# Kernel tuning notes

Hardware: AMD Instinct MI355X
Metric: run time of the kernel (lower is better)

Reference implementation:

```python
import jax, jax.numpy as jnp
import numpy as np

WINDOW = 4
EPS = 1e-5


def setup_inputs() -> dict:
    key = jax.random.key(0)
    ks = jax.random.split(key, 12)
    B, T, D = 2, 4096, 1024
    H = D // 2
    s = 0.02
    return {
        "x": jax.random.normal(ks[0], (B, T, D), dtype=jnp.float32),
        # tension_net: Linear(2D -> D/2), SiLU, Linear(D/2 -> 1). Weights stored [in, out].
        "w1": jax.random.normal(ks[1], (2 * D, H), dtype=jnp.float32) * s,
        "b1": jnp.zeros((H,), dtype=jnp.float32),
        "w2": jax.random.normal(ks[2], (H, 1), dtype=jnp.float32) * s,
        "b2": jnp.zeros((1,), dtype=jnp.float32),
        # wv: Linear(D -> D)
        "wv_w": jax.random.normal(ks[3], (D, D), dtype=jnp.float32) * s,
        "wv_b": jnp.zeros((D,), dtype=jnp.float32),
        # merge: Linear(2D -> D)
        "merge_w": jax.random.normal(ks[4], (2 * D, D), dtype=jnp.float32) * s,
        "merge_b": jnp.zeros((D,), dtype=jnp.float32),
        # LayerNorm(D)
        "gamma": jnp.ones((D,), dtype=jnp.float32),
        "beta": jnp.zeros((D,), dtype=jnp.float32),
    }


def reference(x, w1, b1, w2, b2, wv_w, wv_b, merge_w, merge_b, gamma, beta):
    B, T, D = x.shape
    W = WINDOW
    # Causal sliding-window neighbor gather: nb[:, t, w] = x[:, t-w-1] if t-w-1 >= 0 else 0.
    idx = jnp.arange(T)[:, None] - jnp.arange(W)[None, :] - 1          # [T, W]
    valid = (idx >= 0)                                                  # [T, W]
    nb = jnp.take(x, jnp.clip(idx, 0, None), axis=1)                   # [B, T, W, D]
    nb = jnp.where(valid[None, :, :, None], nb, jnp.zeros((), x.dtype))
    # Pairwise tension gate: tiny MLP on [h_t, nb].
    h_t = jnp.broadcast_to(x[:, :, None, :], (B, T, W, D))
    pair = jnp.concatenate([h_t, nb], axis=-1)                          # [B, T, W, 2D]
    hid = jax.nn.silu(jnp.einsum('btwe,eh->btwh', pair, w1) + b1)       # [B, T, W, D/2]
    tau = jax.nn.sigmoid((jnp.einsum('btwh,ho->btwo', hid, w2) + b2)[..., 0])  # [B, T, W]
    # Value projection of neighbors (note: zero-padded neighbors still get wv bias, matching torch).
    v = jnp.einsum('btwd,de->btwe', nb, wv_w) + wv_b                    # [B, T, W, D]
    msg = jnp.einsum('btw,btwd->btd', tau, v)                           # [B, T, D]
    # Merge + LayerNorm.
    y = jnp.einsum('bte,ed->btd', jnp.concatenate([x, msg], axis=-1), merge_w) + merge_b
    mu = jnp.mean(y, axis=-1, keepdims=True)
    var = jnp.mean(jnp.square(y - mu), axis=-1, keepdims=True)
    y = (y - mu) * jax.lax.rsqrt(var + EPS) * gamma + beta
    return y
```

## Files before the change

### kernel.cpp

```cpp
#include <hip/hip_runtime.h>
#include <hip/hip_bf16.h>

#define TT 4096
#define TD 1024
#define TM 8192
#define CN 3072
#define EPS 1e-5f

typedef __bf16 bf16;
typedef __bf16 bf16x4 __attribute__((ext_vector_type(4)));
typedef __bf16 bf16x8 __attribute__((ext_vector_type(8)));
typedef float  f32x4  __attribute__((ext_vector_type(4)));

#define GLOBAL_AS __attribute__((address_space(1)))
#define LDS_AS    __attribute__((address_space(3)))

__global__ __launch_bounds__(256) void prep_kernel(const float* __restrict__ x,
                                                   const float* __restrict__ w1,
                                                   const float* __restrict__ wv_w,
                                                   const float* __restrict__ wv_b,
                                                   const float* __restrict__ merge_w,
                                                   bf16* __restrict__ Xbf,
                                                   bf16* __restrict__ BigBT,
                                                   bf16* __restrict__ Amb,
                                                   bf16* __restrict__ WvBf,
                                                   float* __restrict__ cvecP) {
    __shared__ float tile[32][33];
    int b = blockIdx.x;
    const int tid = threadIdx.x;

    if (b < 16) {
        const int j = (b & 3) * 256 + tid;
        const int e0 = (b >> 2) * 256;
        const float* col = merge_w + (size_t)(1024 + e0) * 1024 + j;
        float acc = 0.f;
#pragma unroll 32
        for (int e = 0; e < 256; ++e) acc += wv_b[e0 + e] * col[(size_t)e * 1024];
        cvecP[(b >> 2) * 1024 + j] = acc;
        return;
    }
    b -= 16;
    if (b < 8192) {
        int i = b * 256 + tid;
        float4 v = ((const float4*)x)[i];
        bf16x4 o; o[0] = (bf16)v.x; o[1] = (bf16)v.y; o[2] = (bf16)v.z; o[3] = (bf16)v.w;
        *(bf16x4*)(Xbf + (size_t)i * 4) = o;
        return;
    }
    b -= 8192;

    const float* src; bf16* dst; int srcN, tilesX, dstOff;
    if (b < 512)       {            src = w1;                        srcN = 512;  tilesX = 16; dst = BigBT; dstOff = 0;    }
    else if (b < 1024) { b -= 512;  src = w1 + (size_t)1024 * 512;   srcN = 512;  tilesX = 16; dst = BigBT; dstOff = 512;  }
    else if (b < 2048) { b -= 1024; src = merge_w;                   srcN = 1024; tilesX = 32; dst = BigBT; dstOff = 2048; }
    else if (b < 3072) { b -= 2048; src = merge_w + (size_t)1024 * 1024; srcN = 1024; tilesX = 32; dst = Amb; dstOff = 0; }
    else {
        b -= 3072;
        int i = b * 256 + tid;
        float4 v = ((const float4*)wv_w)[i];
        bf16x4 o; o[0] = (bf16)v.x; o[1] = (bf16)v.y; o[2] = (bf16)v.z; o[3] = (bf16)v.w;
        *(bf16x4*)(WvBf + (size_t)i * 4) = o;
        return;
    }
    int n0 = (b % tilesX) * 32, k0 = (b / tilesX) * 32;
    int tx = tid & 31, ty = tid >> 5;
#pragma unroll
    for (int r = 0; r < 32; r += 8)
        tile[ty + r][tx] = src[(size_t)(k0 + ty + r) * srcN + n0 + tx];
    __syncthreads();
#pragma unroll
    for (int r = 0; r < 32; r += 8)
        dst[(size_t)(dstOff + n0 + ty + r) * 1024 + k0 + tx] = (bf16)tile[tx][ty + r];
}

__global__ __launch_bounds__(256) void wprime_kernel(const bf16* __restrict__ Amb,
                                                     const bf16* __restrict__ WvBf,
                                                     bf16* __restrict__ Wout,
                                                     const float* __restrict__ cvecP,
                                                     float* __restrict__ cvec) {
    int b = blockIdx.x;
    if (b == 256) {
        int j = threadIdx.x * 4;
        float4 s0 = *(const float4*)(cvecP + j);
        float4 s1 = *(const float4*)(cvecP + 1024 + j);
        float4 s2 = *(const float4*)(cvecP + 2048 + j);
        float4 s3 = *(const float4*)(cvecP + 3072 + j);
        float4 o = {s0.x + s1.x + s2.x + s3.x, s0.y + s1.y + s2.y + s3.y,
                    s0.z + s1.z + s2.z + s3.z, s0.w + s1.w + s2.w + s3.w};
        *(float4*)(cvec + j) = o;
        return;
    }
    __shared__ bf16 As[64 * 64];
    __shared__ bf16 Bs[64 * 64];
    const int m0 = (b >> 4) * 64;
    const int n0 = (b & 15) * 64;
    const int tid = threadIdx.x;
    const int wave = tid >> 6, lane = tid & 63;
    const int wr = (wave >> 1) * 32, wc = (wave & 1) * 32;
    const int lrow = lane & 15, cbase = lane >> 4;
    const int sw = lrow & 7;

    f32x4 acc[2][2] = {};

    for (int k0 = 0; k0 < 1024; k0 += 64) {
        __syncthreads();
#pragma unroll
        for (int c = 0; c < 2; ++c) {
            int e = (c * 256 + tid) * 8;
            int row = e >> 6;
            int q = (e >> 3) & 7;
            int gcol = ((q ^ (row & 7)) << 3);
            const bf16* ga = Amb  + (size_t)(m0 + row) * 1024 + k0 + gcol;
            const bf16* gb = WvBf + (size_t)(n0 + row) * 1024 + k0 + gcol;
            __builtin_amdgcn_global_load_lds((const GLOBAL_AS void*)ga,
                                             (LDS_AS void*)(As + e), 16, 0, 0);
            __builtin_amdgcn_global_load_lds((const GLOBAL_AS void*)gb,
                                             (LDS_AS void*)(Bs + e), 16, 0, 0);
        }
        __syncthreads();

#pragma unroll
        for (int kk = 0; kk < 2; ++kk) {
            const int qo = ((cbase + kk * 4) ^ sw) << 3;
            bf16x8 af[2], bfr[2];
#pragma unroll
            for (int i = 0; i < 2; ++i) {
                af[i]  = *(const bf16x8*)(As + (wr + i * 16 + lrow) * 64 + qo);
                bfr[i] = *(const bf16x8*)(Bs + (wc + i * 16 + lrow) * 64 + qo);
            }
#pragma unroll
            for (int i = 0; i < 2; ++i)
#pragma unroll
                for (int j = 0; j < 2; ++j)
                    acc[i][j] = __builtin_amdgcn_mfma_f32_16x16x32_bf16(af[i], bfr[j], acc[i][j], 0, 0, 0);
        }
    }

    const int lr = (lane >> 4) * 4, lc = lane & 15;
#pragma unroll
    for (int i = 0; i < 2; ++i)
#pragma unroll
        for (int j = 0; j < 2; ++j)
#pragma unroll
            for (int r = 0; r < 4; ++r)
                Wout[(size_t)(m0 + wr + i * 16 + lr + r) * 1024 + (n0 + wc + j * 16 + lc)]
                    = (bf16)acc[i][j][r];
}

__global__ __launch_bounds__(256, 2) void gemm_big(const bf16* __restrict__ A,
                                                   const bf16* __restrict__ BT,
                                                   bf16* __restrict__ C) {
    __shared__ bf16 SMEM[28672];
    bf16* As = SMEM;
    bf16* Bs = SMEM + 16384;
    const int NB = 3072, K = 1024;

    int bx = blockIdx.x, by = blockIdx.y;
    {
        int L = by * 32 + bx;
        int xcd = L & 7, idx = L >> 3;
        by = xcd * 4 + (idx >> 5);
        bx = idx & 31;
    }
    const int m0 = by * 256;
    const int n0 = bx * 96;
    const int tid = threadIdx.x;
    const int wave = tid >> 6, lane = tid & 63;
    const int wr = wave * 64;
    const int lrow = lane & 15, cbase = lane >> 4;
    const int sw = lrow & 7;

    f32x4 acc[4][6] = {};

    for (int k0 = 0; k0 < K; k0 += 64) {
        __syncthreads();
#pragma unroll
        for (int c = 0; c < 11; ++c) {
            if (c < 8) {
                int e = (c * 256 + tid) * 8;
                int row = e >> 6;
                int q = (e >> 3) & 7;
                int gcol = ((q ^ (row & 7)) << 3);
                const bf16* ga = A + (size_t)(m0 + row) * K + k0 + gcol;
                __builtin_amdgcn_global_load_lds((const GLOBAL_AS void*)ga,
                                                 (LDS_AS void*)(As + e), 16, 0, 0);
            } else {
                int e = ((c - 8) * 256 + tid) * 8;
                int row = e >> 6;
                int q = (e >> 3) & 7;
                int gcol = ((q ^ (row & 7)) << 3);
                const bf16* gb = BT + (size_t)(n0 + row) * K + k0 + gcol;
                __builtin_amdgcn_global_load_lds((const GLOBAL_AS void*)gb,
                                                 (LDS_AS void*)(Bs + e), 16, 0, 0);
            }
        }
        __syncthreads();

#pragma unroll
        for (int kk = 0; kk < 2; ++kk) {
            const int qo = ((cbase + kk * 4) ^ sw) << 3;
            bf16x8 af[4], bfr[6];
#pragma unroll
            for (int i = 0; i < 4; ++i)
                af[i] = *(const bf16x8*)(As + (wr + i * 16 + lrow) * 64 + qo);
#pragma unroll
            for (int j = 0; j < 6; ++j)
                bfr[j] = *(const bf16x8*)(Bs + (j * 16 + lrow) * 64 + qo);
#pragma unroll
            for (int i = 0; i < 4; ++i)
#pragma unroll
                for (int j = 0; j < 6; ++j)
                    acc[i][j] = __builtin_amdgcn_mfma_f32_16x16x32_bf16(af[i], bfr[j], acc[i][j], 0, 0, 0);
        }
    }

    __syncthreads();
    bf16* ep = SMEM + wave * 6656;
    const int lr = (lane >> 4) * 4, lc = lane & 15;
#pragma unroll
    for (int i = 0; i < 4; ++i)
#pragma unroll
        for (int j = 0; j < 6; ++j)
#pragma unroll
            for (int r = 0; r < 4; ++r)
                ep[(i * 16 + lr + r) * 104 + (j * 16 + lc)] = (bf16)acc[i][j][r];
    __syncthreads();

    bf16* Cw = C + (size_t)(m0 + wr) * NB + n0;
#pragma unroll
    for (int p = 0; p < 8; ++p) {
        int R = p * 8 + (lane >> 3);
        int Ccol = (lane & 7) * 8;
        bf16x8 v = *(const bf16x8*)(ep + R * 104 + Ccol);
        *(bf16x8*)(Cw + (size_t)R * NB + Ccol) = v;
    }
#pragma unroll
    for (int p = 0; p < 4; ++p) {
        int R = p * 16 + (lane >> 2);
        int Ccol = 64 + (lane & 3) * 8;
        bf16x8 v = *(const bf16x8*)(ep + R * 104 + Ccol);
        *(bf16x8*)(Cw + (size_t)R * NB + Ccol) = v;
    }
}

__global__ __launch_bounds__(256) void final_kernel(const bf16* __restrict__ C,
                                                    const float* __restrict__ b1,
                                                    const float* __restrict__ b2,
                                                    const float* __restrict__ w2,
                                                    const float* __restrict__ cvec,
                                                    const float* __restrict__ merge_b,
                                                    const float* __restrict__ gamma,
                                                    const float* __restrict__ beta,
                                                    float* __restrict__ out) {
    const int wave = threadIdx.x >> 6, lane = threadIdx.x & 63;
    const int row = blockIdx.x * 4 + wave;
    const int t = row & (TT - 1);
    const bf16* Crow = C + (size_t)row * CN;

    const int h0 = lane * 8;
    bf16x8 u8 = *(const bf16x8*)(Crow + h0);
    float4 b1a = *(const float4*)(b1 + h0), b1b = *(const float4*)(b1 + h0 + 4);
    float4 w2a = *(const float4*)(w2 + h0), w2b = *(const float4*)(w2 + h0 + 4);
    float u[8] = {(float)u8[0] + b1a.x, (float)u8[1] + b1a.y,
                  (float)u8[2] + b1a.z, (float)u8[3] + b1a.w,
                  (float)u8[4] + b1b.x, (float)u8[5] + b1b.y,
                  (float)u8[6] + b1b.z, (float)u8[7] + b1b.w};
    const float w2v[8] = {w2a.x, w2a.y, w2a.z, w2a.w, w2b.x, w2b.y, w2b.z, w2b.w};

    float partial[4];
#pragma unroll
    for (int w = 0; w < 4; ++w) {
        float p = 0.f;
        if (t >= w + 1) {
            bf16x8 v8 = *(const bf16x8*)(C + (size_t)(row - w - 1) * CN + 512 + h0);
#pragma unroll
            for (int k = 0; k < 8; ++k) {
                float z = u[k] + (float)v8[k];
                p += (z / (1.f + __expf(-z))) * w2v[k];
            }
        } else {
#pragma unroll
            for (int k = 0; k < 8; ++k) {
                float z = u[k];
                p += (z / (1.f + __expf(-z))) * w2v[k];
            }
        }
        partial[w] = p;
    }
#pragma unroll
    for (int w = 0; w < 4; ++w)
#pragma unroll
        for (int off = 1; off < 64; off <<= 1)
            partial[w] += __shfl_xor(partial[w], off, 64);

    const float bias2 = b2[0];
    float taus[4];
#pragma unroll
    for (int w = 0; w < 4; ++w)
        taus[w] = 1.f / (1.f + __expf(-(partial[w] + bias2)));
    const float tsum = taus[0] + taus[1] + taus[2] + taus[3];

    const int d0 = lane * 16;
    bf16x8 y1a = *(const bf16x8*)(Crow + 2048 + d0);
    bf16x8 y1b = *(const bf16x8*)(Crow + 2048 + d0 + 8);
    float v[16];
#pragma unroll
    for (int k = 0; k < 8; ++k) { v[k] = (float)y1a[k]; v[8 + k] = (float)y1b[k]; }
#pragma unroll
    for (int q = 0; q < 4; ++q) {
        float4 cv = *(const float4*)(cvec + d0 + q * 4);
        float4 mb = *(const float4*)(merge_b + d0 + q * 4);
        v[q*4+0] += tsum * cv.x + mb.x; v[q*4+1] += tsum * cv.y + mb.y;
        v[q*4+2] += tsum * cv.z + mb.z; v[q*4+3] += tsum * cv.w + mb.w;
    }
#pragma unroll
    for (int w = 0; w < 4; ++w) {
        if (t >= w + 1) {
            const bf16* Pn = C + (size_t)(row - w - 1) * CN + 1024 + d0;
            bf16x8 pa = *(const bf16x8*)Pn;
            bf16x8 pb = *(const bf16x8*)(Pn + 8);
#pragma unroll
            for (int k = 0; k < 8; ++k) {
                v[k] += taus[w] * (float)pa[k];
                v[8 + k] += taus[w] * (float)pb[k];
            }
        }
    }

    float s = 0.f, ss = 0.f;
#pragma unroll
    for (int k = 0; k < 16; ++k) { s += v[k]; ss += v[k] * v[k]; }
#pragma unroll
    for (int off = 1; off < 64; off <<= 1) {
        s  += __shfl_xor(s, off, 64);
        ss += __shfl_xor(ss, off, 64);
    }
    const float mu = s * (1.f / TD);
    const float var = ss * (1.f / TD) - mu * mu;
    const float r = rsqrtf(var + EPS);

#pragma unroll
    for (int q = 0; q < 4; ++q) {
        float4 g  = *(const float4*)(gamma + d0 + q * 4);
        float4 bt = *(const float4*)(beta + d0 + q * 4);
        float4 o;
        o.x = (v[q*4+0] - mu) * r * g.x + bt.x;
        o.y = (v[q*4+1] - mu) * r * g.y + bt.y;
        o.z = (v[q*4+2] - mu) * r * g.z + bt.z;
        o.w = (v[q*4+3] - mu) * r * g.w + bt.w;
        *(float4*)(out + (size_t)row * TD + d0 + q * 4) = o;
    }
}

extern "C" void kernel_launch(void* const* d_in, const int* in_sizes, int n_in,
                              void* d_out, int out_size, void* d_ws, size_t ws_size,
                              hipStream_t stream) {
    const float* x       = (const float*)d_in[0];
    const float* w1      = (const float*)d_in[1];
    const float* b1      = (const float*)d_in[2];
    const float* w2      = (const float*)d_in[3];
    const float* b2      = (const float*)d_in[4];
    const float* wv_w    = (const float*)d_in[5];
    const float* wv_b    = (const float*)d_in[6];
    const float* merge_w = (const float*)d_in[7];
    const float* merge_b = (const float*)d_in[8];
    const float* gamma   = (const float*)d_in[9];
    const float* beta    = (const float*)d_in[10];
    float* out = (float*)d_out;

    char* ws = (char*)d_ws;
    bf16*  Xbf   = (bf16*)ws;  ws += (size_t)TM * 1024 * 2;
    bf16*  BigBT = (bf16*)ws;  ws += (size_t)CN * 1024 * 2;
    bf16*  Amb   = (bf16*)ws;  ws += (size_t)1024 * 1024 * 2;
    bf16*  WvBf  = (bf16*)ws;  ws += (size_t)1024 * 1024 * 2;
    float* cvecP = (float*)ws; ws += (size_t)4 * 1024 * 4;
    float* cvec  = (float*)ws; ws += (size_t)1024 * 4;
    bf16*  Cbuf  = (bf16*)ws;

    prep_kernel<<<12304, 256, 0, stream>>>(x, w1, wv_w, wv_b, merge_w,
                                           Xbf, BigBT, Amb, WvBf, cvecP);

    wprime_kernel<<<257, 256, 0, stream>>>(Amb, WvBf, BigBT + (size_t)1024 * 1024,
                                           cvecP, cvec);

    gemm_big<<<dim3(32, 32), 256, 0, stream>>>(Xbf, BigBT, Cbuf);

    final_kernel<<<TM / 4, 256, 0, stream>>>(Cbuf, b1, b2, w2, cvec, merge_b,
                                             gamma, beta, out);
}
```

Baseline: 195.1 us.

## Fuse all stages into one cooperative persistent kernel with grid syncs

Merges the prep, weight-product, main GEMM and final LayerNorm stages into a single cooperative kernel of 512 persistent blocks that loop over work units, with grid-wide barriers between stages. The cvec partial-sum reduction now happens inside the final stage, so the separate reduction block goes away. The aim is to remove the gaps between kernel launches. In exchange, every stage shares one 56KB LDS allocation and a fixed grid, which may lower occupancy for the light stages, and grid.sync adds its own cost. A fallback to separate launches is kept in case the cooperative launch fails.

New measurement: 409.8 us. 110% more time.

```diff
diff --git a/kernel.cpp b/kernel.cpp
--- a/kernel.cpp
+++ b/kernel.cpp
@@ -1,5 +1,8 @@
 #include <hip/hip_runtime.h>
 #include <hip/hip_bf16.h>
+#include <hip/hip_cooperative_groups.h>
+
+namespace cg = cooperative_groups;
 
 #define TT 4096
 #define TD 1024
@@ -15,20 +18,18 @@
 #define GLOBAL_AS __attribute__((address_space(1)))
 #define LDS_AS    __attribute__((address_space(3)))
 
-__global__ __launch_bounds__(256) void prep_kernel(const float* __restrict__ x,
-                                                   const float* __restrict__ w1,
-                                                   const float* __restrict__ wv_w,
-                                                   const float* __restrict__ wv_b,
-                                                   const float* __restrict__ merge_w,
-                                                   bf16* __restrict__ Xbf,
-                                                   bf16* __restrict__ BigBT,
-                                                   bf16* __restrict__ Amb,
-                                                   bf16* __restrict__ WvBf,
-                                                   float* __restrict__ cvecP) {
-    __shared__ float tile[32][33];
-    int b = blockIdx.x;
+__device__ __forceinline__ void prep_unit(int b, char* smem,
+                                          const float* __restrict__ x,
+                                          const float* __restrict__ w1,
+                                          const float* __restrict__ wv_w,
+                                          const float* __restrict__ wv_b,
+                                          const float* __restrict__ merge_w,
+                                          bf16* __restrict__ Xbf,
+                                          bf16* __restrict__ BigBT,
+                                          bf16* __restrict__ Amb,
+                                          bf16* __restrict__ WvBf,
+                                          float* __restrict__ cvecP) {
     const int tid = threadIdx.x;
-
     if (b < 16) {
         const int j = (b & 3) * 256 + tid;
         const int e0 = (b >> 2) * 256;
@@ -48,20 +49,19 @@
         return;
     }
     b -= 8192;
-
-    const float* src; bf16* dst; int srcN, tilesX, dstOff;
-    if (b < 512)       {            src = w1;                        srcN = 512;  tilesX = 16; dst = BigBT; dstOff = 0;    }
-    else if (b < 1024) { b -= 512;  src = w1 + (size_t)1024 * 512;   srcN = 512;  tilesX = 16; dst = BigBT; dstOff = 512;  }
-    else if (b < 2048) { b -= 1024; src = merge_w;                   srcN = 1024; tilesX = 32; dst = BigBT; dstOff = 2048; }
-    else if (b < 3072) { b -= 2048; src = merge_w + (size_t)1024 * 1024; srcN = 1024; tilesX = 32; dst = Amb; dstOff = 0; }
-    else {
-        b -= 3072;
-        int i = b * 256 + tid;
+    if (b >= 3072) {
+        int i = (b - 3072) * 256 + tid;
         float4 v = ((const float4*)wv_w)[i];
         bf16x4 o; o[0] = (bf16)v.x; o[1] = (bf16)v.y; o[2] = (bf16)v.z; o[3] = (bf16)v.w;
         *(bf16x4*)(WvBf + (size_t)i * 4) = o;
         return;
     }
+    const float* src; bf16* dst; int srcN, tilesX, dstOff;
+    if (b < 512)       {           src = w1;                        srcN = 512;  tilesX = 16; dst = BigBT; dstOff = 0;    }
+    else if (b < 1024) { b -= 512; src = w1 + (size_t)1024 * 512;   srcN = 512;  tilesX = 16; dst = BigBT; dstOff = 512;  }
+    else if (b < 2048) { b -= 1024; src = merge_w;                  srcN = 1024; tilesX = 32; dst = BigBT; dstOff = 2048; }
+    else               { b -= 2048; src = merge_w + (size_t)1024 * 1024; srcN = 1024; tilesX = 32; dst = Amb; dstOff = 0; }
+    float (*tile)[33] = (float(*)[33])smem;
     int n0 = (b % tilesX) * 32, k0 = (b / tilesX) * 32;
     int tx = tid & 31, ty = tid >> 5;
 #pragma unroll
@@ -71,27 +71,15 @@
 #pragma unroll
     for (int r = 0; r < 32; r += 8)
         dst[(size_t)(dstOff + n0 + ty + r) * 1024 + k0 + tx] = (bf16)tile[tx][ty + r];
-}
-
-__global__ __launch_bounds__(256) void wprime_kernel(const bf16* __restrict__ Amb,
-                                                     const bf16* __restrict__ WvBf,
-                                                     bf16* __restrict__ Wout,
-                                                     const float* __restrict__ cvecP,
-                                                     float* __restrict__ cvec) {
-    int b = blockIdx.x;
-    if (b == 256) {
-        int j = threadIdx.x * 4;
-        float4 s0 = *(const float4*)(cvecP + j);
-        float4 s1 = *(const float4*)(cvecP + 1024 + j);
-        float4 s2 = *(const float4*)(cvecP + 2048 + j);
-        float4 s3 = *(const float4*)(cvecP + 3072 + j);
-        float4 o = {s0.x + s1.x + s2.x + s3.x, s0.y + s1.y + s2.y + s3.y,
-                    s0.z + s1.z + s2.z + s3.z, s0.w + s1.w + s2.w + s3.w};
-        *(float4*)(cvec + j) = o;
-        return;
-    }
-    __shared__ bf16 As[64 * 64];
-    __shared__ bf16 Bs[64 * 64];
+    __syncthreads();
+}
+
+__device__ __forceinline__ void wprime_unit(int b, char* smem,
+                                            const bf16* __restrict__ Amb,
+                                            const bf16* __restrict__ WvBf,
+                                            bf16* __restrict__ Wout) {
+    bf16* As = (bf16*)smem;
+    bf16* Bs = (bf16*)smem + 4096;
     const int m0 = (b >> 4) * 64;
     const int n0 = (b & 15) * 64;
     const int tid = threadIdx.x;
@@ -135,6 +123,7 @@
                     acc[i][j] = __builtin_amdgcn_mfma_f32_16x16x32_bf16(af[i], bfr[j], acc[i][j], 0, 0, 0);
         }
     }
+    __syncthreads();
 
     const int lr = (lane >> 4) * 4, lc = lane & 15;
 #pragma unroll
@@ -147,21 +136,17 @@
                     = (bf16)acc[i][j][r];
 }
 
-__global__ __launch_bounds__(256, 2) void gemm_big(const bf16* __restrict__ A,
-                                                   const bf16* __restrict__ BT,
-                                                   bf16* __restrict__ C) {
-    __shared__ bf16 SMEM[28672];
-    bf16* As = SMEM;
-    bf16* Bs = SMEM + 16384;
+__device__ __forceinline__ void gemm_tile(int tb, char* smem,
+                                          const bf16* __restrict__ A,
+                                          const bf16* __restrict__ BT,
+                                          bf16* __restrict__ C) {
+    bf16* As = (bf16*)smem;
+    bf16* Bs = (bf16*)smem + 16384;
     const int NB = 3072, K = 1024;
 
-    int bx = blockIdx.x, by = blockIdx.y;
-    {
-        int L = by * 32 + bx;
-        int xcd = L & 7, idx = L >> 3;
-        by = xcd * 4 + (idx >> 5);
-        bx = idx & 31;
-    }
+    const int xcd = tb & 7, idx = tb >> 3;
+    const int by = xcd * 4 + (idx >> 5);
+    const int bx = idx & 31;
     const int m0 = by * 256;
     const int n0 = bx * 96;
     const int tid = threadIdx.x;
@@ -215,7 +200,7 @@
     }
 
     __syncthreads();
-    bf16* ep = SMEM + wave * 6656;
+    bf16* ep = (bf16*)smem + wave * 6656;
     const int lr = (lane >> 4) * 4, lc = lane & 15;
 #pragma unroll
     for (int i = 0; i < 4; ++i)
@@ -243,17 +228,18 @@
     }
 }
 
-__global__ __launch_bounds__(256) void final_kernel(const bf16* __restrict__ C,
-                                                    const float* __restrict__ b1,
-                                                    const float* __restrict__ b2,
-                                                    const float* __restrict__ w2,
-                                                    const float* __restrict__ cvec,
-                                                    const float* __restrict__ merge_b,
-                                                    const float* __restrict__ gamma,
-                                                    const float* __restrict__ beta,
-                                                    float* __restrict__ out) {
+__device__ __forceinline__ void final_unit(int b,
+                                           const bf16* __restrict__ C,
+                                           const float* __restrict__ b1,
+                                           const float* __restrict__ b2,
+                                           const float* __restrict__ w2,
+                                           const float* __restrict__ cvecP,
+                                           const float* __restrict__ merge_b,
+                                           const float* __restrict__ gamma,
+                                           const float* __restrict__ beta,
+                                           float* __restrict__ out) {
     const int wave = threadIdx.x >> 6, lane = threadIdx.x & 63;
-    const int row = blockIdx.x * 4 + wave;
+    const int row = b * 4 + wave;
     const int t = row & (TT - 1);
     const bf16* Crow = C + (size_t)row * CN;
 
@@ -308,10 +294,16 @@
     for (int k = 0; k < 8; ++k) { v[k] = (float)y1a[k]; v[8 + k] = (float)y1b[k]; }
 #pragma unroll
     for (int q = 0; q < 4; ++q) {
-        float4 cv = *(const float4*)(cvec + d0 + q * 4);
-        float4 mb = *(const float4*)(merge_b + d0 + q * 4);
-        v[q*4+0] += tsum * cv.x + mb.x; v[q*4+1] += tsum * cv.y + mb.y;
-        v[q*4+2] += tsum * cv.z + mb.z; v[q*4+3] += tsum * cv.w + mb.w;
+        const int d = d0 + q * 4;
+        float4 c0 = *(const float4*)(cvecP + d);
+        float4 c1 = *(const float4*)(cvecP + 1024 + d);
+        float4 c2 = *(const float4*)(cvecP + 2048 + d);
+        float4 c3 = *(const float4*)(cvecP + 3072 + d);
+        float4 mb = *(const float4*)(merge_b + d);
+        v[q*4+0] += tsum * (c0.x + c1.x + c2.x + c3.x) + mb.x;
+        v[q*4+1] += tsum * (c0.y + c1.y + c2.y + c3.y) + mb.y;
+        v[q*4+2] += tsum * (c0.z + c1.z + c2.z + c3.z) + mb.z;
+        v[q*4+3] += tsum * (c0.w + c1.w + c2.w + c3.w) + mb.w;
     }
 #pragma unroll
     for (int w = 0; w < 4; ++w) {
@@ -341,15 +333,68 @@
 
 #pragma unroll
     for (int q = 0; q < 4; ++q) {
-        float4 g  = *(const float4*)(gamma + d0 + q * 4);
-        float4 bt = *(const float4*)(beta + d0 + q * 4);
+        const int d = d0 + q * 4;
+        float4 g  = *(const float4*)(gamma + d);
+        float4 bt = *(const float4*)(beta + d);
         float4 o;
         o.x = (v[q*4+0] - mu) * r * g.x + bt.x;
         o.y = (v[q*4+1] - mu) * r * g.y + bt.y;
         o.z = (v[q*4+2] - mu) * r * g.z + bt.z;
         o.w = (v[q*4+3] - mu) * r * g.w + bt.w;
-        *(float4*)(out + (size_t)row * TD + d0 + q * 4) = o;
-    }
+        *(float4*)(out + (size_t)row * TD + d) = o;
+    }
+}
+
+__global__ __launch_bounds__(256, 2) void mega_kernel(
+        const float* x, const float* w1, const float* b1, const float* w2,
+        const float* b2, const float* wv_w, const float* wv_b,
+        const float* merge_w, const float* merge_b, const float* gamma,
+        const float* beta, bf16* Xbf, bf16* BigBT, bf16* Amb, bf16* WvBf,
+        float* cvecP, bf16* Cbuf, float* out) {
+    cg::grid_group grid = cg::this_grid();
+    __shared__ __align__(16) char smem[57344];
+
+    for (int b = blockIdx.x; b < 12304; b += 512)
+        prep_unit(b, smem, x, w1, wv_w, wv_b, merge_w, Xbf, BigBT, Amb, WvBf, cvecP);
+    grid.sync();
+
+    if (blockIdx.x < 256)
+        wprime_unit(blockIdx.x, smem, Amb, WvBf, BigBT + (size_t)1024 * 1024);
+    grid.sync();
+
+    for (int tb = blockIdx.x; tb < 1024; tb += 512)
+        gemm_tile(tb, smem, Xbf, BigBT, Cbuf);
+    grid.sync();
+
+    for (int b = blockIdx.x; b < 2048; b += 512)
+        final_unit(b, Cbuf, b1, b2, w2, cvecP, merge_b, gamma, beta, out);
+}
+
+__global__ __launch_bounds__(256) void prep_kernel(
+        const float* x, const float* w1, const float* wv_w, const float* wv_b,
+        const float* merge_w, bf16* Xbf, bf16* BigBT, bf16* Amb, bf16* WvBf,
+        float* cvecP) {
+    __shared__ __align__(16) char smem[4224];
+    prep_unit(blockIdx.x, smem, x, w1, wv_w, wv_b, merge_w, Xbf, BigBT, Amb, WvBf, cvecP);
+}
+
+__global__ __launch_bounds__(256) void wprime_kernel(
+        const bf16* Amb, const bf16* WvBf, bf16* Wout) {
+    __shared__ __align__(16) char smem[16384];
+    wprime_unit(blockIdx.x, smem, Amb, WvBf, Wout);
+}
+
+__global__ __launch_bounds__(256, 2) void gemm_kernel(
+        const bf16* A, const bf16* BT, bf16* C) {
+    __shared__ __align__(16) char smem[57344];
+    gemm_tile(blockIdx.x, smem, A, BT, C);
+}
+
+__global__ __launch_bounds__(256) void final_kernel(
+        const bf16* C, const float* b1, const float* b2, const float* w2,
+        const float* cvecP, const float* merge_b, const float* gamma,
+        const float* beta, float* out) {
+    final_unit(blockIdx.x, C, b1, b2, w2, cvecP, merge_b, gamma, beta, out);
 }
 
 extern "C" void kernel_launch(void* const* d_in, const int* in_sizes, int n_in,
@@ -374,17 +419,23 @@
     bf16*  Amb   = (bf16*)ws;  ws += (size_t)1024 * 1024 * 2;
     bf16*  WvBf  = (bf16*)ws;  ws += (size_t)1024 * 1024 * 2;
     float* cvecP = (float*)ws; ws += (size_t)4 * 1024 * 4;
-    float* cvec  = (float*)ws; ws += (size_t)1024 * 4;
     bf16*  Cbuf  = (bf16*)ws;
 
-    prep_kernel<<<12304, 256, 0, stream>>>(x, w1, wv_w, wv_b, merge_w,
-                                           Xbf, BigBT, Amb, WvBf, cvecP);
-
-    wprime_kernel<<<257, 256, 0, stream>>>(Amb, WvBf, BigBT + (size_t)1024 * 1024,
-                                           cvecP, cvec);
-
-    gemm_big<<<dim3(32, 32), 256, 0, stream>>>(Xbf, BigBT, Cbuf);
-
-    final_kernel<<<TM / 4, 256, 0, stream>>>(Cbuf, b1, b2, w2, cvec, merge_b,
-                                             gamma, beta, out);
-}
+    void* args[] = {(void*)&x, (void*)&w1, (void*)&b1, (void*)&w2, (void*)&b2,
+                    (void*)&wv_w, (void*)&wv_b, (void*)&merge_w, (void*)&merge_b,
+                    (void*)&gamma, (void*)&beta,
+                    (void*)&Xbf, (void*)&BigBT, (void*)&Amb, (void*)&WvBf,
+                    (void*)&cvecP, (void*)&Cbuf, (void*)&out};
+    hipError_t err = hipLaunchCooperativeKernel((void*)mega_kernel,
+                                                dim3(512), dim3(256),
+                                                args, 0, stream);
+    if (err != hipSuccess) {
+        (void)hipGetLastError();
+        prep_kernel<<<12304, 256, 0, stream>>>(x, w1, wv_w, wv_b, merge_w,
+                                               Xbf, BigBT, Amb, WvBf, cvecP);
+        wprime_kernel<<<256, 256, 0, stream>>>(Amb, WvBf, BigBT + (size_t)1024 * 1024);
+        gemm_kernel<<<1024, 256, 0, stream>>>(Xbf, BigBT, Cbuf);
+        final_kernel<<<2048, 256, 0, stream>>>(Cbuf, b1, b2, w2, cvecP, merge_b,
+                                               gamma, beta, out);
+    }
+}
```

## Rebalance prep work: move x conversion and cvec partials into wprime GEMM launch

Applied to the files above, without the earlier changes.

Weight transposes stay in the prep kernel. The x-to-bf16 conversion and the wv_b·merge_w partial sums move into the W' GEMM launch, so that small GEMM overlaps with bandwidth-bound conversion blocks and the prep kernel shrinks. The final cvec reduction is folded into final_kernel, which now reads the four partials directly. Other changes: the big GEMM uses a 1D grid, one epilogue barrier is dropped, and final_kernel rows are remapped for XCD locality. Removing the barrier after the per-wave LDS epilogue relies on each wave reading back only its own region.

Result: slower. 200.8 us (+2.9%).

```diff
diff --git a/kernel.cpp b/kernel.cpp
--- a/kernel.cpp
+++ b/kernel.cpp
@@ -15,21 +15,54 @@
 #define GLOBAL_AS __attribute__((address_space(1)))
 #define LDS_AS    __attribute__((address_space(3)))
 
-__global__ __launch_bounds__(256) void prep_kernel(const float* __restrict__ x,
-                                                   const float* __restrict__ w1,
+__global__ __launch_bounds__(256) void prep_kernel(const float* __restrict__ w1,
                                                    const float* __restrict__ wv_w,
-                                                   const float* __restrict__ wv_b,
                                                    const float* __restrict__ merge_w,
-                                                   bf16* __restrict__ Xbf,
                                                    bf16* __restrict__ BigBT,
                                                    bf16* __restrict__ Amb,
-                                                   bf16* __restrict__ WvBf,
-                                                   float* __restrict__ cvecP) {
+                                                   bf16* __restrict__ WvBf) {
     __shared__ float tile[32][33];
     int b = blockIdx.x;
     const int tid = threadIdx.x;
 
-    if (b < 16) {
+    if (b >= 3072) {
+        int i = (b - 3072) * 256 + tid;
+        float4 v = ((const float4*)wv_w)[i];
+        bf16x4 o; o[0] = (bf16)v.x; o[1] = (bf16)v.y; o[2] = (bf16)v.z; o[3] = (bf16)v.w;
+        *(bf16x4*)(WvBf + (size_t)i * 4) = o;
+        return;
+    }
+    const float* src; bf16* dst; int srcN, tilesX, dstOff;
+    if (b < 512)       {            src = w1;                        srcN = 512;  tilesX = 16; dst = BigBT; dstOff = 0;    }
+    else if (b < 1024) { b -= 512;  src = w1 + (size_t)1024 * 512;   srcN = 512;  tilesX = 16; dst = BigBT; dstOff = 512;  }
+    else if (b < 2048) { b -= 1024; src = merge_w;                   srcN = 1024; tilesX = 32; dst = BigBT; dstOff = 2048; }
+    else               { b -= 2048; src = merge_w + (size_t)1024 * 1024; srcN = 1024; tilesX = 32; dst = Amb; dstOff = 0; }
+    int n0 = (b % tilesX) * 32, k0 = (b / tilesX) * 32;
+    int tx = tid & 31, ty = tid >> 5;
+#pragma unroll
+    for (int r = 0; r < 32; r += 8)
+        tile[ty + r][tx] = src[(size_t)(k0 + ty + r) * srcN + n0 + tx];
+    __syncthreads();
+#pragma unroll
+    for (int r = 0; r < 32; r += 8)
+        dst[(size_t)(dstOff + n0 + ty + r) * 1024 + k0 + tx] = (bf16)tile[tx][ty + r];
+}
+
+__global__ __launch_bounds__(256) void aux_kernel(const float* __restrict__ x,
+                                                  const float* __restrict__ merge_w,
+                                                  const float* __restrict__ wv_b,
+                                                  const bf16* __restrict__ Amb,
+                                                  const bf16* __restrict__ WvBf,
+                                                  bf16* __restrict__ Wout,
+                                                  bf16* __restrict__ Xbf,
+                                                  float* __restrict__ cvecP) {
+    __shared__ bf16 As[64 * 64];
+    __shared__ bf16 Bs[64 * 64];
+    int b = blockIdx.x;
+    const int tid = threadIdx.x;
+
+    if (b >= 8448) {
+        b -= 8448;
         const int j = (b & 3) * 256 + tid;
         const int e0 = (b >> 2) * 256;
         const float* col = merge_w + (size_t)(1024 + e0) * 1024 + j;
@@ -39,62 +72,15 @@
         cvecP[(b >> 2) * 1024 + j] = acc;
         return;
     }
-    b -= 16;
-    if (b < 8192) {
-        int i = b * 256 + tid;
+    if (b >= 256) {
+        int i = (b - 256) * 256 + tid;
         float4 v = ((const float4*)x)[i];
         bf16x4 o; o[0] = (bf16)v.x; o[1] = (bf16)v.y; o[2] = (bf16)v.z; o[3] = (bf16)v.w;
         *(bf16x4*)(Xbf + (size_t)i * 4) = o;
         return;
     }
-    b -= 8192;
-
-    const float* src; bf16* dst; int srcN, tilesX, dstOff;
-    if (b < 512)       {            src = w1;                        srcN = 512;  tilesX = 16; dst = BigBT; dstOff = 0;    }
-    else if (b < 1024) { b -= 512;  src = w1 + (size_t)1024 * 512;   srcN = 512;  tilesX = 16; dst = BigBT; dstOff = 512;  }
-    else if (b < 2048) { b -= 1024; src = merge_w;                   srcN = 1024; tilesX = 32; dst = BigBT; dstOff = 2048; }
-    else if (b < 3072) { b -= 2048; src = merge_w + (size_t)1024 * 1024; srcN = 1024; tilesX = 32; dst = Amb; dstOff = 0; }
-    else {
-        b -= 3072;
-        int i = b * 256 + tid;
-        float4 v = ((const float4*)wv_w)[i];
-        bf16x4 o; o[0] = (bf16)v.x; o[1] = (bf16)v.y; o[2] = (bf16)v.z; o[3] = (bf16)v.w;
-        *(bf16x4*)(WvBf + (size_t)i * 4) = o;
-        return;
-    }
-    int n0 = (b % tilesX) * 32, k0 = (b / tilesX) * 32;
-    int tx = tid & 31, ty = tid >> 5;
-#pragma unroll
-    for (int r = 0; r < 32; r += 8)
-        tile[ty + r][tx] = src[(size_t)(k0 + ty + r) * srcN + n0 + tx];
-    __syncthreads();
-#pragma unroll
-    for (int r = 0; r < 32; r += 8)
-        dst[(size_t)(dstOff + n0 + ty + r) * 1024 + k0 + tx] = (bf16)tile[tx][ty + r];
-}
-
-__global__ __launch_bounds__(256) void wprime_kernel(const bf16* __restrict__ Amb,
-                                                     const bf16* __restrict__ WvBf,
-                                                     bf16* __restrict__ Wout,
-                                                     const float* __restrict__ cvecP,
-                                                     float* __restrict__ cvec) {
-    int b = blockIdx.x;
-    if (b == 256) {
-        int j = threadIdx.x * 4;
-        float4 s0 = *(const float4*)(cvecP + j);
-        float4 s1 = *(const float4*)(cvecP + 1024 + j);
-        float4 s2 = *(const float4*)(cvecP + 2048 + j);
-        float4 s3 = *(const float4*)(cvecP + 3072 + j);
-        float4 o = {s0.x + s1.x + s2.x + s3.x, s0.y + s1.y + s2.y + s3.y,
-                    s0.z + s1.z + s2.z + s3.z, s0.w + s1.w + s2.w + s3.w};
-        *(float4*)(cvec + j) = o;
-        return;
-    }
-    __shared__ bf16 As[64 * 64];
-    __shared__ bf16 Bs[64 * 64];
     const int m0 = (b >> 4) * 64;
     const int n0 = (b & 15) * 64;
-    const int tid = threadIdx.x;
     const int wave = tid >> 6, lane = tid & 63;
     const int wr = (wave >> 1) * 32, wc = (wave & 1) * 32;
     const int lrow = lane & 15, cbase = lane >> 4;
@@ -147,21 +133,18 @@
                     = (bf16)acc[i][j][r];
 }
 
-__global__ __launch_bounds__(256, 2) void gemm_big(const bf16* __restrict__ A,
-                                                   const bf16* __restrict__ BT,
-                                                   bf16* __restrict__ C) {
+__global__ __launch_bounds__(256, 2) void gemm_kernel(const bf16* __restrict__ A,
+                                                      const bf16* __restrict__ BT,
+                                                      bf16* __restrict__ C) {
     __shared__ bf16 SMEM[28672];
     bf16* As = SMEM;
     bf16* Bs = SMEM + 16384;
     const int NB = 3072, K = 1024;
 
-    int bx = blockIdx.x, by = blockIdx.y;
-    {
-        int L = by * 32 + bx;
-        int xcd = L & 7, idx = L >> 3;
-        by = xcd * 4 + (idx >> 5);
-        bx = idx & 31;
-    }
+    const int tb = blockIdx.x;
+    const int xcd = tb & 7, idx = tb >> 3;
+    const int by = xcd * 4 + (idx >> 5);
+    const int bx = idx & 31;
     const int m0 = by * 256;
     const int n0 = bx * 96;
     const int tid = threadIdx.x;
@@ -224,7 +207,6 @@
 #pragma unroll
             for (int r = 0; r < 4; ++r)
                 ep[(i * 16 + lr + r) * 104 + (j * 16 + lc)] = (bf16)acc[i][j][r];
-    __syncthreads();
 
     bf16* Cw = C + (size_t)(m0 + wr) * NB + n0;
 #pragma unroll
@@ -247,13 +229,14 @@
                                                     const float* __restrict__ b1,
                                                     const float* __restrict__ b2,
                                                     const float* __restrict__ w2,
-                                                    const float* __restrict__ cvec,
+                                                    const float* __restrict__ cvecP,
                                                     const float* __restrict__ merge_b,
                                                     const float* __restrict__ gamma,
                                                     const float* __restrict__ beta,
                                                     float* __restrict__ out) {
+    const int g = (blockIdx.x & 7) * 256 + (blockIdx.x >> 3);
     const int wave = threadIdx.x >> 6, lane = threadIdx.x & 63;
-    const int row = blockIdx.x * 4 + wave;
+    const int row = g * 4 + wave;
     const int t = row & (TT - 1);
     const bf16* Crow = C + (size_t)row * CN;
 
@@ -308,10 +291,16 @@
     for (int k = 0; k < 8; ++k) { v[k] = (float)y1a[k]; v[8 + k] = (float)y1b[k]; }
 #pragma unroll
     for (int q = 0; q < 4; ++q) {
-        float4 cv = *(const float4*)(cvec + d0 + q * 4);
-        float4 mb = *(const float4*)(merge_b + d0 + q * 4);
-        v[q*4+0] += tsum * cv.x + mb.x; v[q*4+1] += tsum * cv.y + mb.y;
-        v[q*4+2] += tsum * cv.z + mb.z; v[q*4+3] += tsum * cv.w + mb.w;
+        const int d = d0 + q * 4;
+        float4 c0 = *(const float4*)(cvecP + d);
+        float4 c1 = *(const float4*)(cvecP + 1024 + d);
+        float4 c2 = *(const float4*)(cvecP + 2048 + d);
+        float4 c3 = *(const float4*)(cvecP + 3072 + d);
+        float4 mb = *(const float4*)(merge_b + d);
+        v[q*4+0] += tsum * (c0.x + c1.x + c2.x + c3.x) + mb.x;
+        v[q*4+1] += tsum * (c0.y + c1.y + c2.y + c3.y) + mb.y;
+        v[q*4+2] += tsum * (c0.z + c1.z + c2.z + c3.z) + mb.z;
+        v[q*4+3] += tsum * (c0.w + c1.w + c2.w + c3.w) + mb.w;
     }
 #pragma unroll
     for (int w = 0; w < 4; ++w) {
@@ -341,14 +330,15 @@
 
 #pragma unroll
     for (int q = 0; q < 4; ++q) {
-        float4 g  = *(const float4*)(gamma + d0 + q * 4);
-        float4 bt = *(const float4*)(beta + d0 + q * 4);
+        const int d = d0 + q * 4;
+        float4 gm = *(const float4*)(gamma + d);
+        float4 bt = *(const float4*)(beta + d);
         float4 o;
-        o.x = (v[q*4+0] - mu) * r * g.x + bt.x;
-        o.y = (v[q*4+1] - mu) * r * g.y + bt.y;
-        o.z = (v[q*4+2] - mu) * r * g.z + bt.z;
-        o.w = (v[q*4+3] - mu) * r * g.w + bt.w;
-        *(float4*)(out + (size_t)row * TD + d0 + q * 4) = o;
+        o.x = (v[q*4+0] - mu) * r * gm.x + bt.x;
+        o.y = (v[q*4+1] - mu) * r * gm.y + bt.y;
+        o.z = (v[q*4+2] - mu) * r * gm.z + bt.z;
+        o.w = (v[q*4+3] - mu) * r * gm.w + bt.w;
+        *(float4*)(out + (size_t)row * TD + d) = o;
     }
 }
 
@@ -374,17 +364,15 @@
     bf16*  Amb   = (bf16*)ws;  ws += (size_t)1024 * 1024 * 2;
     bf16*  WvBf  = (bf16*)ws;  ws += (size_t)1024 * 1024 * 2;
     float* cvecP = (float*)ws; ws += (size_t)4 * 1024 * 4;
-    float* cvec  = (float*)ws; ws += (size_t)1024 * 4;
     bf16*  Cbuf  = (bf16*)ws;
 
-    prep_kernel<<<12304, 256, 0, stream>>>(x, w1, wv_w, wv_b, merge_w,
-                                           Xbf, BigBT, Amb, WvBf, cvecP);
-
-    wprime_kernel<<<257, 256, 0, stream>>>(Amb, WvBf, BigBT + (size_t)1024 * 1024,
-                                           cvecP, cvec);
-
-    gemm_big<<<dim3(32, 32), 256, 0, stream>>>(Xbf, BigBT, Cbuf);
-
-    final_kernel<<<TM / 4, 256, 0, stream>>>(Cbuf, b1, b2, w2, cvec, merge_b,
-                                             gamma, beta, out);
-}
+    prep_kernel<<<4096, 256, 0, stream>>>(w1, wv_w, merge_w, BigBT, Amb, WvBf);
+
+    aux_kernel<<<8464, 256, 0, stream>>>(x, merge_w, wv_b, Amb, WvBf,
+                                         BigBT + (size_t)1024 * 1024, Xbf, cvecP);
+
+    gemm_kernel<<<1024, 256, 0, stream>>>(Xbf, BigBT, Cbuf);
+
+    final_kernel<<<2048, 256, 0, stream>>>(Cbuf, b1, b2, w2, cvecP, merge_b,
+                                           gamma, beta, out);
+}
```
